# Kernel tuning notes

Measured on AMD Instinct MI355X. Metric: run time of the kernel, lower is better.

Reference implementation:

```python
import jax, jax.numpy as jnp
import numpy as np

HEADS = 8
DIM = 512
DIM_HEAD = DIM // 8        # 64
M = DIM // 2               # 256 landmarks
PINV_ITERS = 6
KERNEL = 33                # residual depthwise conv kernel (33,1)


def moore_penrose_pinv(x, iters):
    # x: [b, h, m, m]; Newton-Schulz style iterative pseudoinverse (lucidrains impl)
    abs_x = jnp.abs(x)
    col = abs_x.sum(axis=-1)
    row = abs_x.sum(axis=-2)
    z = jnp.swapaxes(x, -1, -2) / (jnp.max(col) * jnp.max(row))
    I = jnp.eye(x.shape[-1], dtype=x.dtype)
    for _ in range(iters):
        xz = x @ z
        z = 0.25 * z @ (13.0 * I - xz @ (15.0 * I - xz @ (7.0 * I - xz)))
    return z


def setup_inputs() -> dict:
    key = jax.random.key(0)
    ks = jax.random.split(key, 5)
    b, n, dim = 4, 8192, DIM
    x = jax.random.normal(ks[0], (b, n, dim), dtype=jnp.float32)
    # to_qkv: Linear(dim, 3*inner_dim, bias=False); inner_dim = heads*dim_head = dim
    w_qkv = jax.random.normal(ks[1], (dim, 3 * dim), dtype=jnp.float32) / np.sqrt(dim)
    # to_out: Linear(inner_dim, dim) with bias (dropout = identity in eval)
    w_out = jax.random.normal(ks[2], (dim, dim), dtype=jnp.float32) / np.sqrt(dim)
    b_out = jax.random.normal(ks[3], (dim,), dtype=jnp.float32) * 0.01
    # res_conv: Conv2d(heads, heads, (33,1), padding=(16,0), groups=heads, bias=False)
    conv_w = jax.random.normal(ks[4], (HEADS, 1, KERNEL, 1), dtype=jnp.float32) / np.sqrt(KERNEL)
    return {"x": x, "w_qkv": w_qkv, "w_out": w_out, "b_out": b_out, "conv_w": conv_w}


def nystrom_attention(x, w_qkv, w_out, b_out, conv_w):
    b, n, dim = x.shape
    h, d, m = HEADS, DIM_HEAD, M
    # pad front so seq len divisible by num_landmarks (no-op for n=8192, m=256)
    pad = (m - n % m) % m
    xp = jnp.pad(x, ((0, 0), (pad, 0), (0, 0)))
    np_ = n + pad

    qkv = xp @ w_qkv                                   # [b, np, 3*dim]
    q, k, v = jnp.split(qkv, 3, axis=-1)
    to_heads = lambda t: t.reshape(b, np_, h, d).transpose(0, 2, 1, 3)  # [b,h,np,d]
    q, k, v = to_heads(q), to_heads(k), to_heads(v)
    q = q * (d ** -0.5)

    l = np_ // m                                       # tokens per landmark
    pool = lambda t: t.reshape(b, h, m, l, d).mean(axis=3)  # [b,h,m,d]
    q_l, k_l = pool(q), pool(k)

    attn1 = jax.nn.softmax(jnp.einsum('bhnd,bhmd->bhnm', q, k_l), axis=-1)    # [b,h,np,m]
    attn2 = jax.nn.softmax(jnp.einsum('bhid,bhjd->bhij', q_l, k_l), axis=-1)  # [b,h,m,m]
    attn3 = jax.nn.softmax(jnp.einsum('bhmd,bhnd->bhmn', q_l, k), axis=-1)    # [b,h,m,np]

    attn2_inv = moore_penrose_pinv(attn2, PINV_ITERS)
    out = (attn1 @ attn2_inv) @ (attn3 @ v)            # [b,h,np,d]

    # depthwise conv residual over the sequence axis, per head
    res = jax.lax.conv_general_dilated(
        v, conv_w, window_strides=(1, 1),
        padding=((KERNEL // 2, KERNEL // 2), (0, 0)),
        dimension_numbers=('NCHW', 'OIHW', 'NCHW'),
        feature_group_count=h)
    out = out + res

    out = out.transpose(0, 2, 1, 3).reshape(b, np_, dim)
    out = out @ w_out + b_out
    return out[:, -n:]


def reference(x, w_qkv, w_out, b_out, conv_w):
    return x + nystrom_attention(x, w_qkv, w_out, b_out, conv_w)
```

## Files before the change

kernel.cpp:

```cpp
#include <hip/hip_runtime.h>


#define N_SEQ 8192
#define DMODEL 512
#define NHEAD 8
#define DHEAD 64
#define NLAND 256
#define BH 32

typedef unsigned short u16;
typedef __attribute__((ext_vector_type(8))) short bh8;
typedef __attribute__((ext_vector_type(4))) float fx4;

__device__ __forceinline__ float bf2f(u16 u) { return __uint_as_float(((unsigned)u) << 16); }
__device__ __forceinline__ u16 f2bf(float f) {
    unsigned x = __float_as_uint(f);
    return (u16)((x + 0x7fffu + ((x >> 16) & 1u)) >> 16);
}
__device__ __forceinline__ fx4 mfma16(bh8 a, bh8 b, fx4 c) {
    return __builtin_amdgcn_mfma_f32_16x16x32_bf16(a, b, c, 0, 0, 0);
}
__device__ __forceinline__ void gload16(u16* lds, const u16* g) {
    __builtin_amdgcn_global_load_lds(
        (const __attribute__((address_space(1))) unsigned int*)g,
        (__attribute__((address_space(3))) unsigned int*)lds, 16, 0, 0);
}

__global__ void detect_kernel(const u16* __restrict__ X, unsigned* flag_out)
{
    __shared__ int cnt;
    if (threadIdx.x == 0) cnt = 0;
    __syncthreads();
    u16 u = X[threadIdx.x * 2];
    int e = (u >> 7) & 0xFF;
    int insane = (u != 0) && (e < 90 || e > 140);
    atomicAdd(&cnt, insane);
    __syncthreads();
    if (threadIdx.x == 0) flag_out[0] = (cnt > 64) ? 1u : 0u;
}

__global__ __launch_bounds__(256) void convert4_kernel(
    const void* __restrict__ in, u16* __restrict__ out, int n4, const unsigned* __restrict__ flag)
{
    int i = blockIdx.x * 256 + threadIdx.x;
    if (i >= n4) return;
    if (flag[0]) {
        float4 v = ((const float4*)in)[i];
        ushort4 o;
        o.x = f2bf(v.x); o.y = f2bf(v.y); o.z = f2bf(v.z); o.w = f2bf(v.w);
        ((ushort4*)out)[i] = o;
    } else {
        ((ushort4*)out)[i] = ((const ushort4*)in)[i];
    }
}

__global__ __launch_bounds__(256) void wtrans_kernel(
    const void* __restrict__ in, u16* __restrict__ out, int rows, int cols,
    const unsigned* __restrict__ flag)
{
    int idx = blockIdx.x * 256 + threadIdx.x;
    if (idx >= rows * cols) return;
    int r = idx / cols, c = idx % cols;
    float v = flag[0] ? ((const float*)in)[idx] : bf2f(((const u16*)in)[idx]);
    out[(size_t)c * rows + r] = f2bf(v);
}

__global__ __launch_bounds__(256) void qkv_mfma_kernel(
    const u16* __restrict__ X, const u16* __restrict__ WT,
    u16* __restrict__ Q, u16* __restrict__ K, u16* __restrict__ VT)
{
    __shared__ u16 Xs[128 * 64];
    __shared__ u16 Ws[128 * 64];
    const int tid = threadIdx.x;
    const int wave = tid >> 6, lane = tid & 63;
    const int wrow = (wave >> 1) * 64, wcol = (wave & 1) * 64;
    const int i0 = blockIdx.x * 128;
    const int j0 = blockIdx.y * 128;
    const int la = lane >> 3, lb = lane & 7;
    const int lm = lane & 15, lq = lane >> 4;
    const int sw = lm & 7;
    const int sc = (lb ^ la) * 8;
    fx4 acc[4][4];
#pragma unroll
    for (int a = 0; a < 4; ++a)
#pragma unroll
        for (int b = 0; b < 4; ++b) acc[a][b] = (fx4){0.f, 0.f, 0.f, 0.f};

    for (int k0 = 0; k0 < DMODEL; k0 += 64) {
        __syncthreads();
#pragma unroll
        for (int jj = 0; jj < 4; ++jj) {
            int rb = wave * 32 + jj * 8;
            gload16(Xs + rb * 64, X + (size_t)(i0 + rb + la) * DMODEL + k0 + sc);
            gload16(Ws + rb * 64, WT + (size_t)(j0 + rb + la) * DMODEL + k0 + sc);
        }
        __syncthreads();
#pragma unroll
        for (int ks = 0; ks < 2; ++ks) {
            const int po = ((ks * 4 + lq) ^ sw) * 8;
            bh8 xf[4], wf[4];
#pragma unroll
            for (int im = 0; im < 4; ++im)
                xf[im] = *(const bh8*)(Xs + (wrow + im * 16 + lm) * 64 + po);
#pragma unroll
            for (int in = 0; in < 4; ++in)
                wf[in] = *(const bh8*)(Ws + (wcol + in * 16 + lm) * 64 + po);
#pragma unroll
            for (int im = 0; im < 4; ++im)
#pragma unroll
                for (int in = 0; in < 4; ++in)
                    acc[im][in] = mfma16(wf[in], xf[im], acc[im][in]);
        }
    }
#pragma unroll
    for (int im = 0; im < 4; ++im) {
        int m = i0 + wrow + im * 16 + lm;
        int bb = m >> 13, ns = m & (N_SEQ - 1);
#pragma unroll
        for (int in = 0; in < 4; ++in) {
            int nn = j0 + wcol + in * 16 + (lq << 2);
            int which = nn >> 9;
            int h = (nn >> 6) & 7;
            int d = nn & 63;
            if (which == 2) {
                size_t vb = (size_t)(bb * NHEAD + h) * DHEAD;
#pragma unroll
                for (int cc = 0; cc < 4; ++cc)
                    VT[(vb + d + cc) * N_SEQ + ns] = f2bf(acc[im][in][cc]);
            } else {
                u16* dst = (which == 0) ? Q : K;
                float s = (which == 0) ? 0.125f : 1.f;
                ushort4 o;
                o.x = f2bf(acc[im][in][0] * s); o.y = f2bf(acc[im][in][1] * s);
                o.z = f2bf(acc[im][in][2] * s); o.w = f2bf(acc[im][in][3] * s);
                *(ushort4*)(dst + ((size_t)(bb * NHEAD + h) * N_SEQ + ns) * DHEAD + d) = o;
            }
        }
    }
}

__global__ __launch_bounds__(64) void pool_kernel(
    const u16* __restrict__ Q, const u16* __restrict__ K,
    float* __restrict__ QL, float* __restrict__ KL,
    u16* __restrict__ QLb, u16* __restrict__ KLb)
{
    int m = blockIdx.x, bh = blockIdx.y, d = threadIdx.x;
    size_t base = ((size_t)bh * N_SEQ + m * 32) * DHEAD + d;
    float sq = 0.f, sk = 0.f;
#pragma unroll
    for (int i = 0; i < 32; ++i) {
        sq += bf2f(Q[base + i * DHEAD]);
        sk += bf2f(K[base + i * DHEAD]);
    }
    size_t ob = ((size_t)bh * NLAND + m) * DHEAD + d;
    sq *= (1.f / 32.f); sk *= (1.f / 32.f);
    QL[ob] = sq; KL[ob] = sk;
    QLb[ob] = f2bf(sq); KLb[ob] = f2bf(sk);
}

__global__ __launch_bounds__(256) void attn2_kernel(
    const float* __restrict__ QL, const float* __restrict__ KL, float* __restrict__ A2)
{
    __shared__ float qrow[64];
    __shared__ float red[256];
    int i = blockIdx.x, bh = blockIdx.y, j = threadIdx.x;
    if (j < 64) qrow[j] = QL[((size_t)bh * NLAND + i) * DHEAD + j];
    __syncthreads();
    const float* kr = KL + ((size_t)bh * NLAND + j) * DHEAD;
    float lg = 0.f;
#pragma unroll
    for (int d = 0; d < 64; ++d) lg += qrow[d] * kr[d];
    red[j] = lg; __syncthreads();
    for (int s = 128; s > 0; s >>= 1) { if (j < s) red[j] = fmaxf(red[j], red[j + s]); __syncthreads(); }
    float mx = red[0]; __syncthreads();
    float p = __expf(lg - mx);
    red[j] = p; __syncthreads();
    for (int s = 128; s > 0; s >>= 1) { if (j < s) red[j] += red[j + s]; __syncthreads(); }
    float sum = red[0];
    A2[((size_t)bh * NLAND + i) * NLAND + j] = p / sum;
}

__global__ void init_scal_kernel(unsigned* scal) { if (threadIdx.x < 2) scal[threadIdx.x] = 0u; }

__global__ __launch_bounds__(256) void absmax_kernel(const float* __restrict__ A2, unsigned* scal)
{
    __shared__ float red[256];
    int bh = blockIdx.x, t = threadIdx.x;
    const float* Ab = A2 + (size_t)bh * 65536;
    float cs = 0.f, rs = 0.f;
    for (int j = 0; j < 256; ++j) cs += fabsf(Ab[t * 256 + j]);
    for (int i = 0; i < 256; ++i) rs += fabsf(Ab[i * 256 + t]);
    red[t] = cs; __syncthreads();
    for (int s = 128; s > 0; s >>= 1) { if (t < s) red[t] = fmaxf(red[t], red[t + s]); __syncthreads(); }
    if (t == 0) atomicMax(scal + 0, __float_as_uint(red[0]));
    __syncthreads();
    red[t] = rs; __syncthreads();
    for (int s = 128; s > 0; s >>= 1) { if (t < s) red[t] = fmaxf(red[t], red[t + s]); __syncthreads(); }
    if (t == 0) atomicMax(scal + 1, __float_as_uint(red[0]));
}

__global__ __launch_bounds__(256) void z0_kernel(
    const float* __restrict__ A2, const unsigned* __restrict__ scal,
    u16* __restrict__ zb, u16* __restrict__ zbT, u16* __restrict__ A2b)
{
    float inv = 1.f / (__uint_as_float(scal[0]) * __uint_as_float(scal[1]));
    size_t idx = (size_t)blockIdx.x * 256 + threadIdx.x;
    size_t bh = idx >> 16;
    int r = (int)(idx & 65535);
    int i = r >> 8, j = r & 255;
    float a = A2[idx];
    zb[idx]  = f2bf(A2[(bh << 16) + (size_t)j * 256 + i] * inv);
    zbT[idx] = f2bf(a * inv);
    A2b[idx] = f2bf(a);
}

__global__ __launch_bounds__(256) void bgemm_mfma_kernel(
    const u16* __restrict__ A, const u16* __restrict__ BT,
    u16* __restrict__ Cn, u16* __restrict__ Ct, const u16* __restrict__ E,
    int N, long sB, long sCn, long sCt, float sc, float alpha, float beta, int wn, int wt)
{
    const int tid = threadIdx.x;
    const int wave = tid >> 6, lane = tid & 63;
    const int wm = (wave >> 1) * 32, wnn = (wave & 1) * 32;
    const int i0 = blockIdx.x * 64, j0 = blockIdx.y * 64, bh = blockIdx.z;
    const u16* Ab = A + (size_t)bh * 65536;
    const u16* Bb = BT + (size_t)bh * sB;
    const int lm = lane & 15, lq = lane >> 4;

    bh8 lf[2][8], rf[2][8];
#pragma unroll
    for (int im = 0; im < 2; ++im) {
        const u16* ap = Ab + (size_t)(i0 + wm + im * 16 + lm) * 256 + lq * 8;
#pragma unroll
        for (int ks = 0; ks < 8; ++ks)
            lf[im][ks] = *(const bh8*)(ap + ks * 32);
    }
#pragma unroll
    for (int in = 0; in < 2; ++in) {
        const u16* bp = Bb + (size_t)(j0 + wnn + in * 16 + lm) * 256 + lq * 8;
#pragma unroll
        for (int ks = 0; ks < 8; ++ks)
            rf[in][ks] = *(const bh8*)(bp + ks * 32);
    }
    fx4 acc[2][2];
#pragma unroll
    for (int a = 0; a < 2; ++a)
#pragma unroll
        for (int b = 0; b < 2; ++b) acc[a][b] = (fx4){0.f, 0.f, 0.f, 0.f};
#pragma unroll
    for (int ks = 0; ks < 8; ++ks)
#pragma unroll
        for (int im = 0; im < 2; ++im)
#pragma unroll
            for (int in = 0; in < 2; ++in)
                acc[im][in] = mfma16(lf[im][ks], rf[in][ks], acc[im][in]);

#pragma unroll
    for (int im = 0; im < 2; ++im) {
#pragma unroll
        for (int in = 0; in < 2; ++in) {
            int n = j0 + wnn + in * 16 + lm;
            int m0 = i0 + wm + im * 16 + (lq << 2);
            float c[4];
#pragma unroll
            for (int r = 0; r < 4; ++r) {
                int m = m0 + r;
                float x = beta * acc[im][in][r];
                if (alpha != 0.f)
                    x += alpha * bf2f(E[(size_t)bh * 65536 + (size_t)m * 256 + n]);
                if (m == n) x += sc;
                c[r] = x;
            }
            if (wn) {
#pragma unroll
                for (int r = 0; r < 4; ++r)
                    Cn[(size_t)bh * sCn + (size_t)(m0 + r) * N + n] = f2bf(c[r]);
            }
            if (wt) {
                ushort4 o;
                o.x = f2bf(c[0]); o.y = f2bf(c[1]); o.z = f2bf(c[2]); o.w = f2bf(c[3]);
                *(ushort4*)(Ct + (size_t)bh * sCt + (size_t)n * 256 + m0) = o;
            }
        }
    }
}

__global__ __launch_bounds__(256, 2) void attn3v_mfma_kernel(
    const u16* __restrict__ QLb, const u16* __restrict__ Kb,
    const u16* __restrict__ VTb, u16* __restrict__ PO, float* __restrict__ ML)
{
    __shared__ u16 Ks[64 * 72];
    __shared__ u16 Vs[64 * 72];
    __shared__ u16 Pw[4][64 * 72];
    const int tid = threadIdx.x;
    const int wave = tid >> 6, lane = tid & 63;
    const int q = lane >> 4, l15 = lane & 15;
    const int part = blockIdx.x;
    const int bh = blockIdx.y;
    const int nbase = part * 512;
    const int srow = tid >> 2, scol = (tid & 3) * 16;
    u16* Pp = Pw[wave];
    bh8 qf[4][2];
#pragma unroll
    for (int mt = 0; mt < 4; ++mt)
#pragma unroll
        for (int ks = 0; ks < 2; ++ks)
            qf[mt][ks] = *(const bh8*)(QLb + ((size_t)bh * NLAND + wave * 64 + mt * 16 + l15) * DHEAD + ks * 32 + q * 8);
    float M[4] = {-1e30f, -1e30f, -1e30f, -1e30f};
    float L[4] = {0.f, 0.f, 0.f, 0.f};
    fx4 O[4][4];
#pragma unroll
    for (int mt = 0; mt < 4; ++mt)
#pragma unroll
        for (int dt = 0; dt < 4; ++dt) O[mt][dt] = (fx4){0.f, 0.f, 0.f, 0.f};

    for (int c = 0; c < 8; ++c) {
        const int n0 = nbase + c * 64;
        uint4 k0v = *(const uint4*)(Kb + ((size_t)bh * N_SEQ + n0 + srow) * DHEAD + scol);
        uint4 k1v = *(const uint4*)(Kb + ((size_t)bh * N_SEQ + n0 + srow) * DHEAD + scol + 8);
        uint4 v0v = *(const uint4*)(VTb + ((size_t)bh * DHEAD + srow) * N_SEQ + n0 + scol);
        uint4 v1v = *(const uint4*)(VTb + ((size_t)bh * DHEAD + srow) * N_SEQ + n0 + scol + 8);
        __syncthreads();
        *(uint4*)(Ks + srow * 72 + scol) = k0v;
        *(uint4*)(Ks + srow * 72 + scol + 8) = k1v;
        *(uint4*)(Vs + srow * 72 + scol) = v0v;
        *(uint4*)(Vs + srow * 72 + scol + 8) = v1v;
        __syncthreads();
        fx4 S[4][4];
#pragma unroll
        for (int nt = 0; nt < 4; ++nt)
#pragma unroll
            for (int mt = 0; mt < 4; ++mt) S[nt][mt] = (fx4){0.f, 0.f, 0.f, 0.f};
#pragma unroll
        for (int ks = 0; ks < 2; ++ks) {
            bh8 kf[4];
#pragma unroll
            for (int nt = 0; nt < 4; ++nt)
                kf[nt] = *(const bh8*)(Ks + (nt * 16 + l15) * 72 + ks * 32 + q * 8);
#pragma unroll
            for (int nt = 0; nt < 4; ++nt)
#pragma unroll
                for (int mt = 0; mt < 4; ++mt)
                    S[nt][mt] = mfma16(kf[nt], qf[mt][ks], S[nt][mt]);
        }
#pragma unroll
        for (int mt = 0; mt < 4; ++mt) {
            float cm = -1e30f;
#pragma unroll
            for (int nt = 0; nt < 4; ++nt)
#pragma unroll
                for (int r = 0; r < 4; ++r) cm = fmaxf(cm, S[nt][mt][r]);
            cm = fmaxf(cm, __shfl_xor(cm, 16));
            cm = fmaxf(cm, __shfl_xor(cm, 32));
            float Mn = fmaxf(M[mt], cm);
            float al = __expf(M[mt] - Mn);
            M[mt] = Mn;
            L[mt] *= al;
#pragma unroll
            for (int dt = 0; dt < 4; ++dt) {
                O[mt][dt][0] *= al; O[mt][dt][1] *= al;
                O[mt][dt][2] *= al; O[mt][dt][3] *= al;
            }
            float ps = 0.f;
#pragma unroll
            for (int nt = 0; nt < 4; ++nt)
#pragma unroll
                for (int r = 0; r < 4; ++r) {
                    float p = __expf(S[nt][mt][r] - Mn);
                    ps += p;
                    Pp[(mt * 16 + l15) * 72 + nt * 16 + q * 4 + r] = f2bf(p);
                }
            ps += __shfl_xor(ps, 16);
            ps += __shfl_xor(ps, 32);
            L[mt] += ps;
        }
#pragma unroll
        for (int ks = 0; ks < 2; ++ks) {
            bh8 pf[4];
#pragma unroll
            for (int mt = 0; mt < 4; ++mt)
                pf[mt] = *(const bh8*)(Pp + (mt * 16 + l15) * 72 + ks * 32 + q * 8);
#pragma unroll
            for (int dt = 0; dt < 4; ++dt) {
                bh8 vf = *(const bh8*)(Vs + (dt * 16 + l15) * 72 + ks * 32 + q * 8);
#pragma unroll
                for (int mt = 0; mt < 4; ++mt)
                    O[mt][dt] = mfma16(vf, pf[mt], O[mt][dt]);
            }
        }
    }
#pragma unroll
    for (int mt = 0; mt < 4; ++mt) {
        size_t mrow = (size_t)(bh * 16 + part) * NLAND + wave * 64 + mt * 16 + l15;
#pragma unroll
        for (int dt = 0; dt < 4; ++dt) {
            ushort4 o;
            o.x = f2bf(O[mt][dt][0]); o.y = f2bf(O[mt][dt][1]);
            o.z = f2bf(O[mt][dt][2]); o.w = f2bf(O[mt][dt][3]);
            *(ushort4*)(PO + mrow * DHEAD + dt * 16 + q * 4) = o;
        }
        if (q == 0) { ML[mrow * 2] = M[mt]; ML[mrow * 2 + 1] = L[mt]; }
    }
}

__global__ __launch_bounds__(64) void combine_kernel(
    const u16* __restrict__ PO, const float* __restrict__ ML, u16* __restrict__ W3VT)
{
    int m = blockIdx.x, bh = blockIdx.y, d = threadIdx.x;
    float Mg = -1e30f;
#pragma unroll
    for (int p = 0; p < 16; ++p)
        Mg = fmaxf(Mg, ML[((size_t)(bh * 16 + p) * NLAND + m) * 2]);
    float denom = 0.f, o = 0.f;
#pragma unroll
    for (int p = 0; p < 16; ++p) {
        size_t ix = (size_t)(bh * 16 + p) * NLAND + m;
        float w = __expf(ML[ix * 2] - Mg);
        denom += ML[ix * 2 + 1] * w;
        o += bf2f(PO[ix * DHEAD + d]) * w;
    }
    W3VT[((size_t)bh * DHEAD + d) * NLAND + m] = f2bf(o / denom);
}

__global__ __launch_bounds__(256) void conv_kernel(
    const u16* __restrict__ VT, const u16* __restrict__ CW, u16* __restrict__ RT)
{
    __shared__ float vl[2080];
    __shared__ float cws[33];
    const int tid = threadIdx.x;
    const int c0 = blockIdx.x * 2048;
    const int row = blockIdx.y;
    const int h = (row >> 6) & 7;
    const u16* src = VT + (size_t)row * N_SEQ;
    for (int i = tid; i < 2080; i += 256) {
        int gn = c0 - 16 + i;
        vl[i] = (gn >= 0 && gn < N_SEQ) ? bf2f(src[gn]) : 0.f;
    }
    if (tid < 33) cws[tid] = bf2f(CW[h * 33 + tid]);
    __syncthreads();
    float v[40];
    const int base = tid * 8;
#pragma unroll
    for (int i = 0; i < 40; ++i) v[i] = vl[base + i];
    float s[8];
#pragma unroll
    for (int j = 0; j < 8; ++j) {
        float a = 0.f;
#pragma unroll
        for (int t = 0; t < 33; ++t) a += cws[t] * v[j + t];
        s[j] = a;
    }
    u16* dst = RT + (size_t)row * N_SEQ + c0 + base;
    ushort4 o0, o1;
    o0.x = f2bf(s[0]); o0.y = f2bf(s[1]); o0.z = f2bf(s[2]); o0.w = f2bf(s[3]);
    o1.x = f2bf(s[4]); o1.y = f2bf(s[5]); o1.z = f2bf(s[6]); o1.w = f2bf(s[7]);
    *(ushort4*)dst = o0;
    *(ushort4*)(dst + 4) = o1;
}

__global__ __launch_bounds__(256) void outheads_mfma_kernel(
    const u16* __restrict__ Qb, const u16* __restrict__ KLb,
    const u16* __restrict__ WMT, const u16* __restrict__ RT,
    u16* __restrict__ Y)
{
    __shared__ u16 Pl[64 * 264];
    __shared__ float wmax[4][64];
    __shared__ float wsum[4][64];
    const int tid = threadIdx.x;
    const int wave = tid >> 6, lane = tid & 63;
    const int q = lane >> 4, l15 = lane & 15;
    const int bh = blockIdx.y;
    const int bb = bh >> 3, h = bh & 7;
    const int n0 = blockIdx.x * 64;
    fx4 S[4][4];
#pragma unroll
    for (int a = 0; a < 4; ++a)
#pragma unroll
        for (int b = 0; b < 4; ++b) S[a][b] = (fx4){0.f, 0.f, 0.f, 0.f};
#pragma unroll
    for (int ks = 0; ks < 2; ++ks) {
        bh8 qfr[4];
#pragma unroll
        for (int nt = 0; nt < 4; ++nt)
            qfr[nt] = *(const bh8*)(Qb + ((size_t)bh * N_SEQ + n0 + nt * 16 + l15) * DHEAD + ks * 32 + q * 8);
#pragma unroll
        for (int mt = 0; mt < 4; ++mt) {
            bh8 kf = *(const bh8*)(KLb + ((size_t)bh * NLAND + wave * 64 + mt * 16 + l15) * DHEAD + ks * 32 + q * 8);
#pragma unroll
            for (int nt = 0; nt < 4; ++nt)
                S[nt][mt] = mfma16(qfr[nt], kf, S[nt][mt]);
        }
    }
#pragma unroll
    for (int nt = 0; nt < 4; ++nt)
#pragma unroll
        for (int r = 0; r < 4; ++r) {
            float pm = fmaxf(fmaxf(S[nt][0][r], S[nt][1][r]), fmaxf(S[nt][2][r], S[nt][3][r]));
            pm = fmaxf(pm, __shfl_xor(pm, 1));
            pm = fmaxf(pm, __shfl_xor(pm, 2));
            pm = fmaxf(pm, __shfl_xor(pm, 4));
            pm = fmaxf(pm, __shfl_xor(pm, 8));
            if (l15 == 0) wmax[wave][nt * 16 + q * 4 + r] = pm;
        }
    __syncthreads();
#pragma unroll
    for (int nt = 0; nt < 4; ++nt)
#pragma unroll
        for (int r = 0; r < 4; ++r) {
            int nl = nt * 16 + q * 4 + r;
            float Mf = fmaxf(fmaxf(wmax[0][nl], wmax[1][nl]), fmaxf(wmax[2][nl], wmax[3][nl]));
            float ps = 0.f;
#pragma unroll
            for (int mt = 0; mt < 4; ++mt) {
                float p = __expf(S[nt][mt][r] - Mf);
                ps += p;
                Pl[nl * 264 + wave * 64 + mt * 16 + l15] = f2bf(p);
            }
            ps += __shfl_xor(ps, 1);
            ps += __shfl_xor(ps, 2);
            ps += __shfl_xor(ps, 4);
            ps += __shfl_xor(ps, 8);
            if (l15 == 0) wsum[wave][nl] = ps;
        }
    __syncthreads();
    fx4 O[4];
#pragma unroll
    for (int nt = 0; nt < 4; ++nt) O[nt] = (fx4){0.f, 0.f, 0.f, 0.f};
#pragma unroll
    for (int ks = 0; ks < 8; ++ks) {
        bh8 af = *(const bh8*)(WMT + ((size_t)bh * DHEAD + wave * 16 + l15) * NLAND + ks * 32 + q * 8);
#pragma unroll
        for (int nt = 0; nt < 4; ++nt) {
            bh8 pf = *(const bh8*)(Pl + (size_t)(nt * 16 + l15) * 264 + ks * 32 + q * 8);
            O[nt] = mfma16(af, pf, O[nt]);
        }
    }
#pragma unroll
    for (int nt = 0; nt < 4; ++nt) {
        int nl = nt * 16 + l15;
        float inv = 1.f / (wsum[0][nl] + wsum[1][nl] + wsum[2][nl] + wsum[3][nl]);
        int d0 = wave * 16 + (q << 2);
        fx4 v = O[nt];
#pragma unroll
        for (int c = 0; c < 4; ++c)
            v[c] = v[c] * inv + bf2f(RT[(size_t)(bh * DHEAD + d0 + c) * N_SEQ + n0 + nl]);
        ushort4 o;
        o.x = f2bf(v[0]); o.y = f2bf(v[1]); o.z = f2bf(v[2]); o.w = f2bf(v[3]);
        *(ushort4*)(Y + ((size_t)bb * N_SEQ + n0 + nl) * DMODEL + h * DHEAD + d0) = o;
    }
}

__global__ __launch_bounds__(256) void final_mfma_kernel(
    const u16* __restrict__ Y, const u16* __restrict__ WT,
    const u16* __restrict__ Bias, const u16* __restrict__ X, void* __restrict__ Out,
    const unsigned* __restrict__ flag)
{
    __shared__ u16 Xs[128 * 64];
    __shared__ u16 Ws[128 * 64];
    const int tid = threadIdx.x;
    const int wave = tid >> 6, lane = tid & 63;
    const int wrow = (wave >> 1) * 64, wcol = (wave & 1) * 64;
    const int i0 = blockIdx.x * 128;
    const int j0 = blockIdx.y * 128;
    const int la = lane >> 3, lb = lane & 7;
    const int lm = lane & 15, lq = lane >> 4;
    const int sw = lm & 7;
    const int sc = (lb ^ la) * 8;
    const unsigned isf32 = flag[0];
    fx4 acc[4][4];
#pragma unroll
    for (int a = 0; a < 4; ++a)
#pragma unroll
        for (int b = 0; b < 4; ++b) acc[a][b] = (fx4){0.f, 0.f, 0.f, 0.f};

    for (int k0 = 0; k0 < DMODEL; k0 += 64) {
        __syncthreads();
#pragma unroll
        for (int jj = 0; jj < 4; ++jj) {
            int rb = wave * 32 + jj * 8;
            gload16(Xs + rb * 64, Y + (size_t)(i0 + rb + la) * DMODEL + k0 + sc);
            gload16(Ws + rb * 64, WT + (size_t)(j0 + rb + la) * DMODEL + k0 + sc);
        }
        __syncthreads();
#pragma unroll
        for (int ks = 0; ks < 2; ++ks) {
            const int po = ((ks * 4 + lq) ^ sw) * 8;
            bh8 xf[4], wf[4];
#pragma unroll
            for (int im = 0; im < 4; ++im)
                xf[im] = *(const bh8*)(Xs + (wrow + im * 16 + lm) * 64 + po);
#pragma unroll
            for (int in = 0; in < 4; ++in)
                wf[in] = *(const bh8*)(Ws + (wcol + in * 16 + lm) * 64 + po);
#pragma unroll
            for (int im = 0; im < 4; ++im)
#pragma unroll
                for (int in = 0; in < 4; ++in)
                    acc[im][in] = mfma16(wf[in], xf[im], acc[im][in]);
        }
    }
#pragma unroll
    for (int im = 0; im < 4; ++im) {
        int m = i0 + wrow + im * 16 + lm;
#pragma unroll
        for (int in = 0; in < 4; ++in) {
            int nn = j0 + wcol + in * 16 + (lq << 2);
            ushort4 b4 = *(const ushort4*)(Bias + nn);
            ushort4 x4 = *(const ushort4*)(X + (size_t)m * DMODEL + nn);
            float c0 = acc[im][in][0] + bf2f(b4.x) + bf2f(x4.x);
            float c1 = acc[im][in][1] + bf2f(b4.y) + bf2f(x4.y);
            float c2 = acc[im][in][2] + bf2f(b4.z) + bf2f(x4.z);
            float c3 = acc[im][in][3] + bf2f(b4.w) + bf2f(x4.w);
            if (isf32) {
                *(float4*)((float*)Out + (size_t)m * DMODEL + nn) = make_float4(c0, c1, c2, c3);
            } else {
                ushort4 o;
                o.x = f2bf(c0); o.y = f2bf(c1); o.z = f2bf(c2); o.w = f2bf(c3);
                *(ushort4*)((u16*)Out + (size_t)m * DMODEL + nn) = o;
            }
        }
    }
}

extern "C" void kernel_launch(void* const* d_in, const int* in_sizes, int n_in,
                              void* d_out, int out_size, void* d_ws, size_t ws_size,
                              hipStream_t stream)
{
    (void)in_sizes; (void)n_in; (void)out_size; (void)ws_size;
    char* ws = (char*)d_ws;
    u16*   Xc    = (u16*)(ws + 0);
    u16*   WqkvT = (u16*)(ws + 33554432);
    u16*   WoutT = (u16*)(ws + 35127296);
    u16*   Boutc = (u16*)(ws + 35651584);
    u16*   CWc   = (u16*)(ws + 35652608);
    u16*   Qb    = (u16*)(ws + 35653632);
    u16*   Kb    = (u16*)(ws + 69208064);
    u16*   RT    = (u16*)(ws + 69208064);
    u16*   VTb   = (u16*)(ws + 102762496);
    float* QL    = (float*)(ws + 136316928);
    float* KL    = (float*)(ws + 138414080);
    u16*   QLb   = (u16*)(ws + 140511232);
    u16*   KLb   = (u16*)(ws + 141559808);
    u16*   W3VT  = (u16*)(ws + 142608384);
    u16*   WMT   = (u16*)(ws + 143656960);
    u16*   A2b   = (u16*)(ws + 144705536);
    u16*   zA    = (u16*)(ws + 148899840);
    u16*   zAT   = (u16*)(ws + 153094144);
    float* A2    = (float*)(ws + 157288448);
    u16*   PO    = (u16*)(ws + 157288448);
    float* ML    = (float*)(ws + 174065664);
    u16*   zB    = (u16*)(ws + 165677056);
    u16*   zBT   = (u16*)(ws + 169871360);
    u16*   xz    = (u16*)(ws + 174065664);
    u16*   xzT   = (u16*)(ws + 178259968);
    u16*   t2T   = (u16*)(ws + 182454272);
    u16*   t3T   = (u16*)(ws + 186648576);
    u16*   Yb    = (u16*)(ws + 157288448);
    unsigned* SCAL = (unsigned*)(ws + 190842880);

    detect_kernel<<<1, 256, 0, stream>>>((const u16*)d_in[0], SCAL + 2);
    convert4_kernel<<<16384, 256, 0, stream>>>(d_in[0], Xc, 4194304, SCAL + 2);
    wtrans_kernel<<<3072, 256, 0, stream>>>(d_in[1], WqkvT, 512, 1536, SCAL + 2);
    wtrans_kernel<<<1024, 256, 0, stream>>>(d_in[2], WoutT, 512, 512, SCAL + 2);
    convert4_kernel<<<1, 256, 0, stream>>>(d_in[3], Boutc, 128, SCAL + 2);
    convert4_kernel<<<1, 256, 0, stream>>>(d_in[4], CWc, 66, SCAL + 2);

    qkv_mfma_kernel<<<dim3(256, 12), 256, 0, stream>>>(Xc, WqkvT, Qb, Kb, VTb);
    pool_kernel<<<dim3(256, BH), 64, 0, stream>>>(Qb, Kb, QL, KL, QLb, KLb);
    attn2_kernel<<<dim3(256, BH), 256, 0, stream>>>(QL, KL, A2);
    init_scal_kernel<<<1, 64, 0, stream>>>(SCAL);
    absmax_kernel<<<32, 256, 0, stream>>>(A2, SCAL);
    z0_kernel<<<8192, 256, 0, stream>>>(A2, SCAL, zA, zAT, A2b);

    attn3v_mfma_kernel<<<dim3(16, BH), 256, 0, stream>>>(QLb, Kb, VTb, PO, ML);
    combine_kernel<<<dim3(256, BH), 64, 0, stream>>>(PO, ML, W3VT);
    conv_kernel<<<dim3(4, 2048), 256, 0, stream>>>(VTb, CWc, RT);

    u16 *z = zA, *zT = zAT, *zn = zB, *znT = zBT;
    for (int it = 0; it < 6; ++it) {
        bgemm_mfma_kernel<<<dim3(4, 4, 32), 256, 0, stream>>>(
            A2b, zT, xz, xzT, A2b, 256, 65536, 65536, 65536, 0.f, 0.f, 1.f, 1, 1);
        bgemm_mfma_kernel<<<dim3(4, 4, 32), 256, 0, stream>>>(
            xz, xzT, xz, t2T, xz, 256, 65536, 65536, 65536, 15.f, -7.f, 1.f, 0, 1);
        bgemm_mfma_kernel<<<dim3(4, 4, 32), 256, 0, stream>>>(
            xz, t2T, xz, t3T, xz, 256, 65536, 65536, 65536, 13.f, 0.f, -1.f, 0, 1);
        bgemm_mfma_kernel<<<dim3(4, 4, 32), 256, 0, stream>>>(
            z, t3T, zn, znT, xz, 256, 65536, 65536, 65536, 0.f, 0.f, 0.25f, 1, 1);
        u16* t;
        t = z; z = zn; zn = t;
        t = zT; zT = znT; znT = t;
    }
    bgemm_mfma_kernel<<<dim3(4, 1, 32), 256, 0, stream>>>(
        z, W3VT, WMT, WMT, xz, 64, 16384, 16384, 16384, 0.f, 0.f, 1.f, 0, 1);
    outheads_mfma_kernel<<<dim3(128, BH), 256, 0, stream>>>(Qb, KLb, WMT, RT, Yb);
    final_mfma_kernel<<<dim3(256, 4), 256, 0, stream>>>(Yb, WoutT, Boutc, Xc, d_out, SCAL + 2);
}
```

Baseline: 815.3 us.

## Fuse pinv Newton-Schulz iteration chain into one persistent kernel per head

Replaces the 25 separate batched-GEMM launches of the pseudoinverse iterations, plus the final Z·W3V product, with a single kernel. It uses one 512-thread block per batch-head and keeps the right-hand operand transposed in a 135 KB LDS buffer. Intermediate xz, y and z rows go through global memory but stay within one block, and the 15I/7I/13I combinations are folded into the epilogues. This removes launch overhead and the transposed-output round trips. In exchange only 32 blocks run, which leaves most CUs idle during a serial MFMA-heavy phase. Re-reading global data that the same block just wrote also carries a cache-coherence risk.

```diff
diff --git a/kernel.cpp b/kernel.cpp
--- a/kernel.cpp
+++ b/kernel.cpp
@@ -214,74 +214,171 @@
     A2b[idx] = f2bf(a);
 }
 
-__global__ __launch_bounds__(256) void bgemm_mfma_kernel(
-    const u16* __restrict__ A, const u16* __restrict__ BT,
-    u16* __restrict__ Cn, u16* __restrict__ Ct, const u16* __restrict__ E,
-    int N, long sB, long sCn, long sCt, float sc, float alpha, float beta, int wn, int wt)
-{
+__global__ __launch_bounds__(512, 2) void pinv_chain_kernel(
+    const u16* __restrict__ A2b, u16* __restrict__ Zrow,
+    const u16* __restrict__ Z0T, u16* __restrict__ XZrow, u16* __restrict__ Yrow,
+    const u16* __restrict__ W3VT, u16* __restrict__ WMT)
+{
+    __shared__ u16 TB[256 * 264];
     const int tid = threadIdx.x;
     const int wave = tid >> 6, lane = tid & 63;
-    const int wm = (wave >> 1) * 32, wnn = (wave & 1) * 32;
-    const int i0 = blockIdx.x * 64, j0 = blockIdx.y * 64, bh = blockIdx.z;
-    const u16* Ab = A + (size_t)bh * 65536;
-    const u16* Bb = BT + (size_t)bh * sB;
-    const int lm = lane & 15, lq = lane >> 4;
-
-    bh8 lf[2][8], rf[2][8];
-#pragma unroll
-    for (int im = 0; im < 2; ++im) {
-        const u16* ap = Ab + (size_t)(i0 + wm + im * 16 + lm) * 256 + lq * 8;
-#pragma unroll
-        for (int ks = 0; ks < 8; ++ks)
-            lf[im][ks] = *(const bh8*)(ap + ks * 32);
-    }
-#pragma unroll
-    for (int in = 0; in < 2; ++in) {
-        const u16* bp = Bb + (size_t)(j0 + wnn + in * 16 + lm) * 256 + lq * 8;
-#pragma unroll
-        for (int ks = 0; ks < 8; ++ks)
-            rf[in][ks] = *(const bh8*)(bp + ks * 32);
-    }
-    fx4 acc[2][2];
-#pragma unroll
-    for (int a = 0; a < 2; ++a)
-#pragma unroll
-        for (int b = 0; b < 2; ++b) acc[a][b] = (fx4){0.f, 0.f, 0.f, 0.f};
-#pragma unroll
-    for (int ks = 0; ks < 8; ++ks)
+    const int q = lane >> 4, l15 = lane & 15;
+    const int bh = blockIdx.x;
+    const int row0 = (wave >> 2) * 128;
+    const int col0 = (wave & 3) * 64;
+    const size_t mb = (size_t)bh * 65536;
+    const u16* Xp = A2b + mb;
+    u16* XZp = XZrow + mb;
+    u16* Yp  = Yrow + mb;
+    u16* Zp  = Zrow + mb;
+
+#pragma unroll
+    for (int i = 0; i < 16; ++i) {
+        int c = tid + 512 * i;
+        int r = c >> 5, cc = (c & 31) * 8;
+        *(bh8*)(TB + r * 264 + cc) = *(const bh8*)(Z0T + mb + (size_t)r * 256 + cc);
+    }
+    __syncthreads();
+
+#pragma unroll 1
+    for (int it = 0; it < 6; ++it) {
+#pragma unroll 1
+        for (int step = 0; step < 4; ++step) {
+            const u16* ap = (step == 0) ? Xp : (step == 1) ? XZp : (step == 2) ? Yp : Zp;
+            fx4 acc[8][4];
+#pragma unroll
+            for (int im = 0; im < 8; ++im)
+#pragma unroll
+                for (int nt = 0; nt < 4; ++nt) acc[im][nt] = (fx4){0.f, 0.f, 0.f, 0.f};
+
+#pragma unroll
+            for (int kc = 0; kc < 4; ++kc) {
+                const int k0 = kc * 64;
+                bh8 bf[4][2];
+#pragma unroll
+                for (int nt = 0; nt < 4; ++nt) {
+                    const u16* tb = TB + (col0 + nt * 16 + l15) * 264 + k0 + q * 8;
+                    bf[nt][0] = *(const bh8*)(tb);
+                    bf[nt][1] = *(const bh8*)(tb + 32);
+                }
+                const u16* ar = ap + (size_t)(row0 + l15) * 256 + k0 + q * 8;
+                bh8 a0 = *(const bh8*)(ar);
+                bh8 a1 = *(const bh8*)(ar + 32);
+#pragma unroll
+                for (int im = 0; im < 8; ++im) {
+                    bh8 n0, n1;
+                    if (im < 7) {
+                        const u16* an = ap + (size_t)(row0 + (im + 1) * 16 + l15) * 256 + k0 + q * 8;
+                        n0 = *(const bh8*)(an);
+                        n1 = *(const bh8*)(an + 32);
+                    }
+#pragma unroll
+                    for (int nt = 0; nt < 4; ++nt) {
+                        acc[im][nt] = mfma16(a0, bf[nt][0], acc[im][nt]);
+                        acc[im][nt] = mfma16(a1, bf[nt][1], acc[im][nt]);
+                    }
+                    a0 = n0; a1 = n1;
+                }
+            }
+            __syncthreads();
+
+            if (step == 0 || step == 1) {
+                u16* outp = (step == 0) ? XZp : Yp;
+#pragma unroll
+                for (int im = 0; im < 8; ++im)
+#pragma unroll
+                    for (int nt = 0; nt < 4; ++nt) {
+                        int col = col0 + nt * 16 + l15;
+                        ushort4 t;
+#pragma unroll
+                        for (int r = 0; r < 4; ++r) {
+                            int row = row0 + im * 16 + q * 4 + r;
+                            u16 v = f2bf(acc[im][nt][r]);
+                            outp[(size_t)row * 256 + col] = v;
+                            ((u16*)&t)[r] = v;
+                        }
+                        if (step == 0)
+                            *(ushort4*)(TB + (size_t)col * 264 + row0 + im * 16 + q * 4) = t;
+                    }
+            } else if (step == 2) {
+#pragma unroll
+                for (int im = 0; im < 8; ++im)
+#pragma unroll
+                    for (int nt = 0; nt < 4; ++nt) {
+                        int col = col0 + nt * 16 + l15;
+                        ushort4 t;
+#pragma unroll
+                        for (int r = 0; r < 4; ++r) {
+                            int row = row0 + im * 16 + q * 4 + r;
+                            float xzv = bf2f(XZp[(size_t)row * 256 + col]);
+                            float yv  = bf2f(Yp[(size_t)row * 256 + col]);
+                            float s = 7.f * yv - 15.f * xzv - acc[im][nt][r]
+                                      + ((row == col) ? 13.f : 0.f);
+                            ((u16*)&t)[r] = f2bf(s);
+                        }
+                        *(ushort4*)(TB + (size_t)col * 264 + row0 + im * 16 + q * 4) = t;
+                    }
+            } else {
+#pragma unroll
+                for (int im = 0; im < 8; ++im)
+#pragma unroll
+                    for (int nt = 0; nt < 4; ++nt) {
+                        int col = col0 + nt * 16 + l15;
+                        ushort4 t;
+#pragma unroll
+                        for (int r = 0; r < 4; ++r) {
+                            int row = row0 + im * 16 + q * 4 + r;
+                            u16 v = f2bf(0.25f * acc[im][nt][r]);
+                            Zp[(size_t)row * 256 + col] = v;
+                            ((u16*)&t)[r] = v;
+                        }
+                        *(ushort4*)(TB + (size_t)col * 264 + row0 + im * 16 + q * 4) = t;
+                    }
+            }
+            __syncthreads();
+        }
+    }
+
+    {
+        const int frow0 = wave * 32;
+        const u16* wp = W3VT + (size_t)bh * 16384;
+        fx4 facc[2][4];
 #pragma unroll
         for (int im = 0; im < 2; ++im)
 #pragma unroll
-            for (int in = 0; in < 2; ++in)
-                acc[im][in] = mfma16(lf[im][ks], rf[in][ks], acc[im][in]);
-
-#pragma unroll
-    for (int im = 0; im < 2; ++im) {
-#pragma unroll
-        for (int in = 0; in < 2; ++in) {
-            int n = j0 + wnn + in * 16 + lm;
-            int m0 = i0 + wm + im * 16 + (lq << 2);
-            float c[4];
-#pragma unroll
-            for (int r = 0; r < 4; ++r) {
-                int m = m0 + r;
-                float x = beta * acc[im][in][r];
-                if (alpha != 0.f)
-                    x += alpha * bf2f(E[(size_t)bh * 65536 + (size_t)m * 256 + n]);
-                if (m == n) x += sc;
-                c[r] = x;
-            }
-            if (wn) {
-#pragma unroll
-                for (int r = 0; r < 4; ++r)
-                    Cn[(size_t)bh * sCn + (size_t)(m0 + r) * N + n] = f2bf(c[r]);
-            }
-            if (wt) {
-                ushort4 o;
-                o.x = f2bf(c[0]); o.y = f2bf(c[1]); o.z = f2bf(c[2]); o.w = f2bf(c[3]);
-                *(ushort4*)(Ct + (size_t)bh * sCt + (size_t)n * 256 + m0) = o;
-            }
-        }
+            for (int nt = 0; nt < 4; ++nt) facc[im][nt] = (fx4){0.f, 0.f, 0.f, 0.f};
+#pragma unroll
+        for (int kc = 0; kc < 4; ++kc) {
+            const int k0 = kc * 64;
+            bh8 bf[4][2];
+#pragma unroll
+            for (int nt = 0; nt < 4; ++nt) {
+                const u16* bp = wp + (size_t)(nt * 16 + l15) * 256 + k0 + q * 8;
+                bf[nt][0] = *(const bh8*)(bp);
+                bf[nt][1] = *(const bh8*)(bp + 32);
+            }
+#pragma unroll
+            for (int im = 0; im < 2; ++im) {
+                const u16* ar = Zp + (size_t)(frow0 + im * 16 + l15) * 256 + k0 + q * 8;
+                bh8 a0 = *(const bh8*)(ar);
+                bh8 a1 = *(const bh8*)(ar + 32);
+#pragma unroll
+                for (int nt = 0; nt < 4; ++nt) {
+                    facc[im][nt] = mfma16(a0, bf[nt][0], facc[im][nt]);
+                    facc[im][nt] = mfma16(a1, bf[nt][1], facc[im][nt]);
+                }
+            }
+        }
+#pragma unroll
+        for (int im = 0; im < 2; ++im)
+#pragma unroll
+            for (int nt = 0; nt < 4; ++nt) {
+                int d = nt * 16 + l15;
+                ushort4 t;
+#pragma unroll
+                for (int r = 0; r < 4; ++r) ((u16*)&t)[r] = f2bf(facc[im][nt][r]);
+                *(ushort4*)(WMT + (size_t)bh * 16384 + (size_t)d * 256 + frow0 + im * 16 + q * 4) = t;
+            }
     }
 }
 
@@ -649,12 +746,8 @@
     float* A2    = (float*)(ws + 157288448);
     u16*   PO    = (u16*)(ws + 157288448);
     float* ML    = (float*)(ws + 174065664);
-    u16*   zB    = (u16*)(ws + 165677056);
-    u16*   zBT   = (u16*)(ws + 169871360);
-    u16*   xz    = (u16*)(ws + 174065664);
-    u16*   xzT   = (u16*)(ws + 178259968);
-    u16*   t2T   = (u16*)(ws + 182454272);
-    u16*   t3T   = (u16*)(ws + 186648576);
+    u16*   XZrow = (u16*)(ws + 174065664);
+    u16*   Yrow  = (u16*)(ws + 182454272);
     u16*   Yb    = (u16*)(ws + 157288448);
     unsigned* SCAL = (unsigned*)(ws + 190842880);
 
@@ -676,22 +769,8 @@
     combine_kernel<<<dim3(256, BH), 64, 0, stream>>>(PO, ML, W3VT);
     conv_kernel<<<dim3(4, 2048), 256, 0, stream>>>(VTb, CWc, RT);
 
-    u16 *z = zA, *zT = zAT, *zn = zB, *znT = zBT;
-    for (int it = 0; it < 6; ++it) {
-        bgemm_mfma_kernel<<<dim3(4, 4, 32), 256, 0, stream>>>(
-            A2b, zT, xz, xzT, A2b, 256, 65536, 65536, 65536, 0.f, 0.f, 1.f, 1, 1);
-        bgemm_mfma_kernel<<<dim3(4, 4, 32), 256, 0, stream>>>(
-            xz, xzT, xz, t2T, xz, 256, 65536, 65536, 65536, 15.f, -7.f, 1.f, 0, 1);
-        bgemm_mfma_kernel<<<dim3(4, 4, 32), 256, 0, stream>>>(
-            xz, t2T, xz, t3T, xz, 256, 65536, 65536, 65536, 13.f, 0.f, -1.f, 0, 1);
-        bgemm_mfma_kernel<<<dim3(4, 4, 32), 256, 0, stream>>>(
-            z, t3T, zn, znT, xz, 256, 65536, 65536, 65536, 0.f, 0.f, 0.25f, 1, 1);
-        u16* t;
-        t = z; z = zn; zn = t;
-        t = zT; zT = znT; znT = t;
-    }
-    bgemm_mfma_kernel<<<dim3(4, 1, 32), 256, 0, stream>>>(
-        z, W3VT, WMT, WMT, xz, 64, 16384, 16384, 16384, 0.f, 0.f, 1.f, 0, 1);
+    pinv_chain_kernel<<<32, 512, 0, stream>>>(A2b, zA, zAT, XZrow, Yrow, W3VT, WMT);
+
     outheads_mfma_kernel<<<dim3(128, BH), 256, 0, stream>>>(Qb, KLb, WMT, RT, Yb);
     final_mfma_kernel<<<dim3(256, 4), 256, 0, stream>>>(Yb, WoutT, Boutc, Xc, d_out, SCAL + 2);
 }
```

Result: slower. 1.667 ms (+104.4%).
